# Kernel tuning notes

Hardware: AMD Instinct MI355X
Metric: run time of the kernel (lower is better)

Reference implementation:

```python
import jax, jax.numpy as jnp
import numpy as np

B, N, DIM = 2, 2048, 2048
H, DK, DV = 16, 64, 128
DIM_INNER = (DK + DV) * H  # 3072
EPS = 1e-12  # matches F.normalize clamp_min eps


def l2norm(t):
    n = jnp.linalg.norm(t, axis=-1, keepdims=True)
    return t / jnp.maximum(n, EPS)


def tanh_norm(t):
    n = jnp.linalg.norm(t, axis=-1, keepdims=True)
    return jnp.tanh(n) * (t / jnp.maximum(n, EPS))


def setup_inputs() -> dict:
    key = jax.random.key(0)
    k1, k2, k3, k4 = jax.random.split(key, 4)
    tokens = jax.random.normal(k1, (B, N, DIM), dtype=jnp.float32)
    # Linear weights stored as [in, out] (y = x @ W)
    Wqg = jax.random.normal(k2, (DIM, DIM_INNER), dtype=jnp.float32) * (DIM ** -0.5)
    Wkv = jax.random.normal(k3, (DIM, DIM_INNER), dtype=jnp.float32) * (DIM ** -0.5)
    Wo = jax.random.normal(k4, (DV * H, DIM), dtype=jnp.float32) * ((DV * H) ** -0.5)
    # LearnedScale log_scales, init log(1.0) = 0
    ls_iaw = jnp.zeros((H,), dtype=jnp.float32)  # inverse_acceptance_width (bias=1.0)
    ls_hws = jnp.zeros((H,), dtype=jnp.float32)  # head_wise_scale (bias=0.0)
    return {"tokens": tokens, "Wqg": Wqg, "Wkv": Wkv, "Wo": Wo,
            "ls_iaw": ls_iaw, "ls_hws": ls_hws}


def _split_heads(t):
    # [b, n, h*d] -> [b, h, n, d]
    b, n, _ = t.shape
    return t.reshape(b, n, H, -1).transpose(0, 2, 1, 3)


def reference(tokens, Wqg, Wkv, Wo, ls_iaw, ls_hws):
    qg = _split_heads(tokens @ Wqg)   # [b, h, n, dk+dv]
    kv = _split_heads(tokens @ Wkv)
    queries, gates = qg[..., :DK], qg[..., DK:]
    keys, values = kv[..., :DK], kv[..., DK:]
    queries, keys, values = l2norm(queries), l2norm(keys), l2norm(values)

    sim = jnp.einsum('bhid,bhjd->bhij', queries, keys)
    # r = 1 / (exp(log_scales) + 1)  (LearnedScale bias=1.0)
    r = 1.0 / (jnp.exp(ls_iaw) + 1.0)[None, :, None, None]
    attn = jnp.square(jax.nn.relu(1.0 - r * (1.0 - sim)))
    # NOTE: original code applies causal mask to `sim` AFTER computing `attn`,
    # so the mask has no effect on the output -- replicated faithfully here.
    aggr = jnp.einsum('bhij,bhjd->bhid', attn, values)
    out = tanh_norm(aggr) * jnp.tanh(jax.nn.silu(gates))
    out = out * jnp.exp(ls_hws)[None, :, None, None]  # head_wise_scale, bias=0
    out = out.transpose(0, 2, 1, 3).reshape(tokens.shape[0], tokens.shape[1], H * DV)
    return out @ Wo
```

## Files before the change

### kernel.cpp

```cpp
#include <hip/hip_runtime.h>
#include <hip/hip_bf16.h>
#include <stdint.h>


typedef unsigned short u16;
typedef __bf16 bf16x8 __attribute__((ext_vector_type(8)));
typedef u16 u16x8 __attribute__((ext_vector_type(8)));
typedef float f32x4 __attribute__((ext_vector_type(4)));
typedef float f32x16 __attribute__((ext_vector_type(16)));
typedef int i32x4 __attribute__((ext_vector_type(4)));

#define DEVINL __device__ __forceinline__

DEVINL u16 f2bf(float f) {
  union { float f; uint32_t u; } v; v.f = f;
  uint32_t r = (v.u + 0x7FFFu + ((v.u >> 16) & 1u)) >> 16;
  return (u16)r;
}
DEVINL float bf2f(u16 x) {
  union { uint32_t u; float f; } v; v.u = ((uint32_t)x) << 16;
  return v.f;
}
DEVINL bf16x8 as_bf(u16x8 v) { return __builtin_bit_cast(bf16x8, v); }

typedef const __attribute__((address_space(1))) uint32_t* gptr_t;
typedef __attribute__((address_space(3))) uint32_t* lptr_t;
DEVINL void gload_lds16(const void* g, void* l) {
  __builtin_amdgcn_global_load_lds((gptr_t)g, (lptr_t)l, 16, 0, 0);
}

DEVINL f32x4 mfma16(u16x8 a, u16x8 b, f32x4 c) {
  return __builtin_amdgcn_mfma_f32_16x16x32_bf16(as_bf(a), as_bf(b), c, 0, 0, 0);
}
DEVINL f32x16 mfma32(u16x8 a, u16x8 b, f32x16 c) {
  return __builtin_amdgcn_mfma_f32_32x32x16_bf16(as_bf(a), as_bf(b), c, 0, 0, 0);
}

__global__ void k_cvt(const float* __restrict__ src, u16* __restrict__ dst, int n) {
  int i = (blockIdx.x * blockDim.x + threadIdx.x) * 4;
  int stride = gridDim.x * blockDim.x * 4;
  for (; i < n; i += stride) {
    float4 f = *(const float4*)(src + i);
    ushort4 o;
    o.x = f2bf(f.x); o.y = f2bf(f.y); o.z = f2bf(f.z); o.w = f2bf(f.w);
    *(ushort4*)(dst + i) = o;
  }
}

__global__ void k_cvtT(const float* __restrict__ src, u16* __restrict__ dst, int R, int C) {
  __shared__ float tile[32][33];
  int c0 = blockIdx.x * 32, r0 = blockIdx.y * 32;
  int tc = threadIdx.x & 31, tr = threadIdx.x >> 5;
#pragma unroll
  for (int i = 0; i < 4; i++) {
    int r = tr + i * 8;
    tile[r][tc] = src[(size_t)(r0 + r) * C + c0 + tc];
  }
  __syncthreads();
#pragma unroll
  for (int i = 0; i < 4; i++) {
    int r = tr + i * 8;
    dst[(size_t)(c0 + r) * R + r0 + tc] = f2bf(tile[tc][r]);
  }
}

template <int F32OUT>
__global__ __launch_bounds__(256, 2) void k_gemm(const u16* __restrict__ A,
                                                 const u16* __restrict__ Bt,
                                                 void* __restrict__ Cout,
                                                 int M, int Nt, int K) {
  __shared__ u16 As[128 * 32];
  __shared__ u16 Bs[128 * 32];
  const int tid = threadIdx.x, lane = tid & 63, wid = tid >> 6;
  const int m0 = blockIdx.y * 128, n0 = blockIdx.x * 128;
  const int wm = (wid >> 1) * 64, wn = (wid & 1) * 64;
  const int fr = lane & 15, fc = (lane >> 4) * 8;

  f32x4 acc[4][4] = {};

  const u16* gA = A + (size_t)(m0 + wid * 32 + (lane >> 2)) * K + (lane & 3) * 8;
  const u16* gB = Bt + (size_t)(n0 + wid * 32 + (lane >> 2)) * K + (lane & 3) * 8;
  u16* lA = As + wid * 1024;
  u16* lB = Bs + wid * 1024;
  const size_t rowskip = (size_t)16 * K;

  for (int k0 = 0; k0 < K; k0 += 32) {
    gload_lds16(gA + k0, lA);
    gload_lds16(gA + k0 + rowskip, lA + 512);
    gload_lds16(gB + k0, lB);
    gload_lds16(gB + k0 + rowskip, lB + 512);
    __syncthreads();
    u16x8 a[4], b[4];
#pragma unroll
    for (int mi = 0; mi < 4; mi++) a[mi] = *(const u16x8*)(As + (wm + mi * 16 + fr) * 32 + fc);
#pragma unroll
    for (int ni = 0; ni < 4; ni++) b[ni] = *(const u16x8*)(Bs + (wn + ni * 16 + fr) * 32 + fc);
#pragma unroll
    for (int mi = 0; mi < 4; mi++)
#pragma unroll
      for (int ni = 0; ni < 4; ni++)
        acc[mi][ni] = mfma16(a[mi], b[ni], acc[mi][ni]);
    __syncthreads();
  }

  const int frow = (lane >> 4) * 4;
#pragma unroll
  for (int mi = 0; mi < 4; mi++)
#pragma unroll
    for (int ni = 0; ni < 4; ni++)
#pragma unroll
      for (int j = 0; j < 4; j++) {
        const size_t row = m0 + wm + mi * 16 + frow + j;
        const size_t col = n0 + wn + ni * 16 + fr;
        if (F32OUT) ((float*)Cout)[row * Nt + col] = acc[mi][ni][j];
        else ((u16*)Cout)[row * Nt + col] = f2bf(acc[mi][ni][j]);
      }
}

__global__ __launch_bounds__(256, 4) void k_norm(const u16* __restrict__ qgkv,
                                                 u16* __restrict__ qn, u16* __restrict__ kn,
                                                 u16* __restrict__ vnT, u16* __restrict__ gact) {
  __shared__ u16 vt[128 * 64];
  const int tid = threadIdx.x, lane = tid & 63, wid = tid >> 6;
  const int hb = blockIdx.y;
  const int h = hb & 15, b = hb >> 4;
  const int n0 = blockIdx.x * 64;

  for (int s = 0; s < 16; s++) {
    const int nl = wid * 16 + s;
    const int n = n0 + nl;
    const size_t bn = (size_t)b * 2048 + n;
    const size_t baseq = bn * 6144 + (size_t)h * 192;
    const size_t basek = baseq + 3072;

    float q = bf2f(qgkv[baseq + lane]);
    float g0 = bf2f(qgkv[baseq + 64 + lane]);
    float g1 = bf2f(qgkv[baseq + 128 + lane]);
    float k = bf2f(qgkv[basek + lane]);
    float v0 = bf2f(qgkv[basek + 64 + lane]);
    float v1 = bf2f(qgkv[basek + 128 + lane]);

    float qs = q * q, ks = k * k, vs = v0 * v0 + v1 * v1;
#pragma unroll
    for (int m = 1; m < 64; m <<= 1) {
      qs += __shfl_xor(qs, m);
      ks += __shfl_xor(ks, m);
      vs += __shfl_xor(vs, m);
    }
    float rq = 1.f / fmaxf(sqrtf(qs), 1e-12f);
    float rk = 1.f / fmaxf(sqrtf(ks), 1e-12f);
    float rv = 1.f / fmaxf(sqrtf(vs), 1e-12f);

    qn[((size_t)hb * 2048 + n) * 64 + lane] = f2bf(q * rq);
    kn[((size_t)hb * 2048 + n) * 64 + lane] = f2bf(k * rk);
    float s0 = g0 / (1.f + __expf(-g0));
    float s1 = g1 / (1.f + __expf(-g1));
    gact[((size_t)hb * 2048 + n) * 128 + lane] = f2bf(tanhf(s0));
    gact[((size_t)hb * 2048 + n) * 128 + 64 + lane] = f2bf(tanhf(s1));

    const int d0 = lane, d1 = 64 + lane;
    vt[d0 * 64 + (nl ^ ((d0 & 15) << 2))] = f2bf(v0 * rv);
    vt[d1 * 64 + (nl ^ ((d1 & 15) << 2))] = f2bf(v1 * rv);
  }
  __syncthreads();

#pragma unroll
  for (int p = 0; p < 8; p++) {
    const int d = p * 16 + (tid >> 4);
    const int nq = (tid & 15) * 4;
    const int cb = nq ^ ((d & 15) << 2);
    const int nq2 = (nq & ~12) | ((nq & 4) << 1) | ((nq & 8) >> 1);
    ushort4 o;
    o.x = vt[d * 64 + cb + 0];
    o.y = vt[d * 64 + cb + 1];
    o.z = vt[d * 64 + cb + 2];
    o.w = vt[d * 64 + cb + 3];
    *(ushort4*)(vnT + ((size_t)hb * 128 + d) * 2048 + n0 + nq2) = o;
  }
}

__global__ __launch_bounds__(256, 2) void k_attn(const u16* __restrict__ qn,
                                                 const u16* __restrict__ kn,
                                                 const u16* __restrict__ vnT,
                                                 const u16* __restrict__ gact,
                                                 const float* __restrict__ ls_iaw,
                                                 const float* __restrict__ ls_hws,
                                                 u16* __restrict__ pre_out) {
  extern __shared__ char smem[];
  u16* KsB = (u16*)smem;
  u16* VsB = (u16*)(smem + 16384);
  u16* Os = (u16*)smem;

  const int tid = threadIdx.x, lane = tid & 63, wid = tid >> 6;
  const int bid = blockIdx.y * 16 + blockIdx.x;
  const int bh = (bid & 7) * 4 + ((bid >> 3) & 3);
  const int n0 = (bid >> 5) * 128;
  const int h = bh & 15;
  const int l31 = lane & 31, L = lane >> 5, rb = l31 & 7;
  const float r = 1.f / (__expf(ls_iaw[h]) + 1.f);
  const float c1 = 1.f - r;
  const float whs = __expf(ls_hws[h]);

  const int wq = wid * 32;
  const u16* qrow = qn + ((size_t)bh * 2048 + n0 + wq + l31) * 64;
  u16x8 qf[4];
#pragma unroll
  for (int c = 0; c < 4; c++) qf[c] = *(const u16x8*)(qrow + c * 16 + L * 8);

  f32x16 acc[4] = {};
  const u16* kbase = kn + (size_t)bh * 2048 * 64;
  const u16* vbase = vnT + (size_t)bh * 128 * 2048;

  int ks_goff[2];
#pragma unroll
  for (int i = 0; i < 2; i++) {
    int row = wid * 16 + i * 8 + (lane >> 3);
    ks_goff[i] = row * 64 + (((lane & 7) ^ (row & 7)) << 3);
  }
  int vs_goff[4];
#pragma unroll
  for (int i = 0; i < 4; i++) {
    int row = wid * 32 + i * 8 + (lane >> 3);
    vs_goff[i] = row * 2048 + (((lane & 7) ^ (row & 7)) << 3);
  }

  {
    u16* KsC = KsB + wid * 1024;
    u16* VsC = VsB + wid * 2048;
#pragma unroll
    for (int i = 0; i < 2; i++) gload_lds16(kbase + ks_goff[i], KsC + i * 512);
#pragma unroll
    for (int i = 0; i < 4; i++) gload_lds16(vbase + vs_goff[i], VsC + i * 512);
  }

  int cur = 0;
  for (int t = 0; t < 32; t++) {
    asm volatile("s_waitcnt vmcnt(0) lgkmcnt(0)" ::: "memory");
    __builtin_amdgcn_s_barrier();
    asm volatile("" ::: "memory");

    if (t < 31) {
      const int kv0 = (t + 1) * 64;
      u16* KsC2 = KsB + (cur ^ 1) * 4096 + wid * 1024;
      u16* VsC2 = VsB + (cur ^ 1) * 8192 + wid * 2048;
#pragma unroll
      for (int i = 0; i < 2; i++) gload_lds16(kbase + (size_t)kv0 * 64 + ks_goff[i], KsC2 + i * 512);
#pragma unroll
      for (int i = 0; i < 4; i++) gload_lds16(vbase + (size_t)vs_goff[i] + kv0, VsC2 + i * 512);
    }

    const u16* KsC = KsB + cur * 4096;
    const u16* VsC = VsB + cur * 8192;

    f32x16 sT0 = {}, sT1 = {};
    __builtin_amdgcn_s_setprio(1);
#pragma unroll
    for (int c = 0; c < 4; c++) {
      u16x8 kf0 = *(const u16x8*)(KsC + (0 + l31) * 64 + (((2 * c + L) ^ rb) << 3));
      u16x8 kf1 = *(const u16x8*)(KsC + (32 + l31) * 64 + (((2 * c + L) ^ rb) << 3));
      sT0 = mfma32(kf0, qf[c], sT0);
      sT1 = mfma32(kf1, qf[c], sT1);
    }
    __builtin_amdgcn_s_setprio(0);

    uint32_t w[2][4][2];
#pragma unroll
    for (int m = 0; m < 4; m++)
#pragma unroll
      for (int p = 0; p < 2; p++) {
        float a0 = fmaxf(0.f, fmaf(r, sT0[4 * m + 2 * p], c1));
        float a1 = fmaxf(0.f, fmaf(r, sT0[4 * m + 2 * p + 1], c1));
        float b0 = fmaxf(0.f, fmaf(r, sT1[4 * m + 2 * p], c1));
        float b1 = fmaxf(0.f, fmaf(r, sT1[4 * m + 2 * p + 1], c1));
        w[0][m][p] = (uint32_t)f2bf(a0 * a0) | ((uint32_t)f2bf(a1 * a1) << 16);
        w[1][m][p] = (uint32_t)f2bf(b0 * b0) | ((uint32_t)f2bf(b1 * b1) << 16);
      }

    __builtin_amdgcn_s_setprio(1);
#pragma unroll
    for (int kt = 0; kt < 2; kt++)
#pragma unroll
      for (int pair = 0; pair < 2; pair++) {
        i32x4 pw;
        pw[0] = (int)w[kt][2 * pair][0];
        pw[1] = (int)w[kt][2 * pair][1];
        pw[2] = (int)w[kt][2 * pair + 1][0];
        pw[3] = (int)w[kt][2 * pair + 1][1];
        u16x8 pf = __builtin_bit_cast(u16x8, pw);
        const int chunk = 4 * kt + 2 * pair + L;
#pragma unroll
        for (int dt = 0; dt < 4; dt++) {
          u16x8 vf = *(const u16x8*)(VsC + (dt * 32 + l31) * 64 + ((chunk ^ rb) << 3));
          acc[dt] = mfma32(vf, pf, acc[dt]);
        }
      }
    __builtin_amdgcn_s_setprio(0);
    cur ^= 1;
  }

  float ss = 0.f;
#pragma unroll
  for (int dt = 0; dt < 4; dt++)
#pragma unroll
    for (int e = 0; e < 16; e++) { float x = acc[dt][e]; ss += x * x; }
  ss += __shfl_xor(ss, 32);
  float nn = sqrtf(ss);
  float scale = tanhf(nn) / fmaxf(nn, 1e-12f) * whs;

  __syncthreads();

  const int q = wq + l31;
  const size_t grow = ((size_t)bh * 2048 + n0 + q) * 128;
#pragma unroll
  for (int dt = 0; dt < 4; dt++)
#pragma unroll
    for (int m = 0; m < 4; m++) {
      const int d = dt * 32 + 8 * m + 4 * L;
      ushort4 gv = *(const ushort4*)(gact + grow + d);
      ushort4 o;
      o.x = f2bf(acc[dt][4 * m + 0] * scale * bf2f(gv.x));
      o.y = f2bf(acc[dt][4 * m + 1] * scale * bf2f(gv.y));
      o.z = f2bf(acc[dt][4 * m + 2] * scale * bf2f(gv.z));
      o.w = f2bf(acc[dt][4 * m + 3] * scale * bf2f(gv.w));
      *(ushort4*)(Os + q * 132 + d) = o;
    }
  __syncthreads();

  const int orow = tid >> 1, oc0 = (tid & 1) * 64;
  const size_t obase = ((size_t)(bh >> 4) * 2048 + n0 + orow) * 2048 + (size_t)h * 128 + oc0;
#pragma unroll
  for (int j = 0; j < 16; j++) {
    ushort4 v = *(const ushort4*)(Os + orow * 132 + oc0 + 4 * j);
    *(ushort4*)(pre_out + obase + 4 * j) = v;
  }
}

extern "C" void kernel_launch(void* const* d_in, const int* in_sizes, int n_in,
                              void* d_out, int out_size, void* d_ws, size_t ws_size,
                              hipStream_t stream) {
  (void)in_sizes; (void)n_in; (void)out_size; (void)ws_size;
  const float* tokens = (const float*)d_in[0];
  const float* Wqg = (const float*)d_in[1];
  const float* Wkv = (const float*)d_in[2];
  const float* Wo = (const float*)d_in[3];
  const float* ls_iaw = (const float*)d_in[4];
  const float* ls_hws = (const float*)d_in[5];
  float* out = (float*)d_out;
  char* ws = (char*)d_ws;

  u16* WoT = (u16*)(ws + 0);
  char* regA = ws + 8388608;
  u16* tok_bf = (u16*)(regA);
  u16* WqgkvT = (u16*)(regA + 16777216);
  u16* qn = (u16*)(regA);
  u16* kn = (u16*)(regA + 8388608);
  u16* vnT = (u16*)(regA + 16777216);
  u16* gact = (u16*)(regA + 33554432);
  char* regB = ws + 58720256;
  u16* qgkv_raw = (u16*)(regB);
  u16* pre_out = (u16*)(regB);

  k_cvt<<<4096, 256, 0, stream>>>(tokens, tok_bf, 8388608);
  k_cvtT<<<dim3(96, 64), 256, 0, stream>>>(Wqg, WqgkvT, 2048, 3072);
  k_cvtT<<<dim3(96, 64), 256, 0, stream>>>(Wkv, WqgkvT + (size_t)3072 * 2048, 2048, 3072);
  k_cvtT<<<dim3(64, 64), 256, 0, stream>>>(Wo, WoT, 2048, 2048);

  k_gemm<0><<<dim3(48, 32), 256, 0, stream>>>(tok_bf, WqgkvT, qgkv_raw, 4096, 6144, 2048);

  k_norm<<<dim3(32, 32), 256, 0, stream>>>(qgkv_raw, qn, kn, vnT, gact);

  k_attn<<<dim3(16, 32), 256, 49152, stream>>>(qn, kn, vnT, gact, ls_iaw, ls_hws, pre_out);

  k_gemm<1><<<dim3(16, 32), 256, 0, stream>>>(pre_out, WoT, out, 4096, 2048, 2048);
}
```

Measured before the change: 302.1 us.

## Add 256x256-tile pipelined GEMM for the QG/KV projection

Replaces the QKV projection GEMM with a new kernel that uses 256x256 output tiles, 512 threads and 128 KB of double-buffered LDS. It issues staged direct-to-LDS loads interleaved with quadrant-wise MFMA work, uses a block-index swizzle for L2 locality, and raises wave priority around the MFMA bursts. The larger tiles are meant to raise arithmetic intensity and hide global-load latency behind compute. In exchange, only one block fits per CU and the grid shrinks to 384 blocks, which risks tail imbalance.

```diff
diff --git a/kernel.cpp b/kernel.cpp
--- a/kernel.cpp
+++ b/kernel.cpp
@@ -115,6 +115,118 @@
         if (F32OUT) ((float*)Cout)[row * Nt + col] = acc[mi][ni][j];
         else ((u16*)Cout)[row * Nt + col] = f2bf(acc[mi][ni][j]);
       }
+}
+
+template <int MH, int NH>
+DEVINL void kg_quad(const u16* __restrict__ Ab, const u16* __restrict__ Bb,
+                    f32x4 (&acc)[2][4][2][2], int mq64, int nq32,
+                    int fr, int hi, int rb7) {
+  u16x8 af[4][2], bf[2][2];
+#pragma unroll
+  for (int mi = 0; mi < 4; mi++)
+#pragma unroll
+    for (int kk = 0; kk < 2; kk++) {
+      const int rrow = MH * 128 + mq64 + mi * 16 + fr;
+      af[mi][kk] = *(const u16x8*)(Ab + rrow * 64 + (((kk * 4 + hi) ^ rb7) << 3));
+    }
+#pragma unroll
+  for (int ni = 0; ni < 2; ni++)
+#pragma unroll
+    for (int kk = 0; kk < 2; kk++) {
+      const int rrow = NH * 128 + nq32 + ni * 16 + fr;
+      bf[ni][kk] = *(const u16x8*)(Bb + rrow * 64 + (((kk * 4 + hi) ^ rb7) << 3));
+    }
+  __builtin_amdgcn_s_setprio(1);
+#pragma unroll
+  for (int kk = 0; kk < 2; kk++)
+#pragma unroll
+    for (int mi = 0; mi < 4; mi++)
+#pragma unroll
+      for (int ni = 0; ni < 2; ni++)
+        acc[MH][mi][NH][ni] = mfma16(af[mi][kk], bf[ni][kk], acc[MH][mi][NH][ni]);
+  __builtin_amdgcn_s_setprio(0);
+}
+
+__global__ __launch_bounds__(512, 1) void k_gemm256(const u16* __restrict__ A,
+                                                    const u16* __restrict__ Bt,
+                                                    u16* __restrict__ C,
+                                                    int Nt, int K) {
+  extern __shared__ char smem[];
+  u16* As = (u16*)smem;
+  u16* Bs = (u16*)(smem + 65536);
+  const int tid = threadIdx.x, lane = tid & 63, wid = tid >> 6;
+
+  const int nbx = Nt >> 8;
+  const int cpx = gridDim.x >> 3;
+  const int bid = blockIdx.x;
+  const int swz = (bid & 7) * cpx + (bid >> 3);
+  const int m0 = (swz / nbx) << 8, n0 = (swz % nbx) << 8;
+
+  const int mq64 = (wid >> 2) * 64, nq32 = (wid & 3) * 32;
+  const int fr = lane & 15, hi = lane >> 4, frow = hi * 4, rb7 = fr & 7;
+
+  f32x4 acc[2][4][2][2] = {};
+
+  const int schunk = ((lane & 7) ^ ((lane >> 3) & 7)) << 3;
+  const int srow = wid * 8 + (lane >> 3);
+  const u16* ga0 = A + (size_t)(m0 + srow) * K + schunk;
+  const u16* gb0 = Bt + (size_t)(n0 + srow) * K + schunk;
+  const size_t l64 = (size_t)64 * K;
+  const int dwave = wid * 8 * 64;
+
+#define SA(P, L, KT) gload_lds16(ga0 + (size_t)(L) * l64 + (KT), As + (P) * 16384 + (L) * 4096 + dwave)
+#define SB(P, L, KT) gload_lds16(gb0 + (size_t)(L) * l64 + (KT), Bs + (P) * 16384 + (L) * 4096 + dwave)
+
+  SA(0, 0, 0); SA(0, 1, 0);
+  SB(0, 0, 0); SB(0, 1, 0);
+  SB(0, 2, 0); SB(0, 3, 0);
+  SA(0, 2, 0); SA(0, 3, 0);
+
+  const int NTI = K >> 6;
+  for (int t = 0; t < NTI; t++) {
+    const int p = t & 1, pn = p ^ 1;
+    const int ktn = (t < NTI - 1 ? t + 1 : t) << 6;
+    const u16* Ab = As + p * 16384;
+    const u16* Bb = Bs + p * 16384;
+
+    asm volatile("s_waitcnt vmcnt(4)" ::: "memory");
+    __builtin_amdgcn_s_barrier();
+    asm volatile("" ::: "memory");
+    SA(pn, 0, ktn); SA(pn, 1, ktn);
+    kg_quad<0, 0>(Ab, Bb, acc, mq64, nq32, fr, hi, rb7);
+
+    asm volatile("s_waitcnt vmcnt(4)" ::: "memory");
+    __builtin_amdgcn_s_barrier();
+    asm volatile("" ::: "memory");
+    SB(pn, 0, ktn); SB(pn, 1, ktn);
+    kg_quad<0, 1>(Ab, Bb, acc, mq64, nq32, fr, hi, rb7);
+
+    asm volatile("s_waitcnt vmcnt(4)" ::: "memory");
+    __builtin_amdgcn_s_barrier();
+    asm volatile("" ::: "memory");
+    SB(pn, 2, ktn); SB(pn, 3, ktn);
+    kg_quad<1, 0>(Ab, Bb, acc, mq64, nq32, fr, hi, rb7);
+
+    SA(pn, 2, ktn); SA(pn, 3, ktn);
+    kg_quad<1, 1>(Ab, Bb, acc, mq64, nq32, fr, hi, rb7);
+  }
+#undef SA
+#undef SB
+
+#pragma unroll
+  for (int mh = 0; mh < 2; mh++)
+#pragma unroll
+    for (int mi = 0; mi < 4; mi++)
+#pragma unroll
+      for (int nh = 0; nh < 2; nh++)
+#pragma unroll
+        for (int ni = 0; ni < 2; ni++)
+#pragma unroll
+          for (int j = 0; j < 4; j++) {
+            const size_t row = m0 + mh * 128 + mq64 + mi * 16 + frow + j;
+            const size_t col = n0 + nh * 128 + nq32 + ni * 16 + fr;
+            C[row * Nt + col] = f2bf(acc[mh][mi][nh][ni][j]);
+          }
 }
 
 __global__ __launch_bounds__(256, 4) void k_norm(const u16* __restrict__ qgkv,
@@ -365,7 +477,7 @@
   k_cvtT<<<dim3(96, 64), 256, 0, stream>>>(Wkv, WqgkvT + (size_t)3072 * 2048, 2048, 3072);
   k_cvtT<<<dim3(64, 64), 256, 0, stream>>>(Wo, WoT, 2048, 2048);
 
-  k_gemm<0><<<dim3(48, 32), 256, 0, stream>>>(tok_bf, WqgkvT, qgkv_raw, 4096, 6144, 2048);
+  k_gemm256<<<384, 512, 131072, stream>>>(tok_bf, WqgkvT, qgkv_raw, 6144, 2048);
 
   k_norm<<<dim3(32, 32), 256, 0, stream>>>(qgkv_raw, qn, kn, vnT, gact);
 
```

After: 303.9 us. About the same (+0.6%).

## Replace GEMM with larger-tile triple-buffered pipelined kernel with swizzle and XCD mapping

Applied to the files above, without the earlier changes.

Replaces the single-buffered 128x128 GEMM with a templated 512-thread kernel that uses larger block tiles (256x384 and 128x256). It triple-buffers LDS with async global-to-LDS loads issued two stages ahead, and waits on partial vmcnt. It also XOR-swizzles the LDS layout to reduce bank conflicts, maps blocks to XCDs for L2 locality, and raises wave priority around the MFMA work. Both projection GEMMs now run as one wave of 256 blocks, which costs occupancy and adds register pressure.

```diff
diff --git a/kernel.cpp b/kernel.cpp
--- a/kernel.cpp
+++ b/kernel.cpp
@@ -64,50 +64,95 @@
   }
 }
 
-template <int F32OUT>
-__global__ __launch_bounds__(256, 2) void k_gemm(const u16* __restrict__ A,
-                                                 const u16* __restrict__ Bt,
-                                                 void* __restrict__ Cout,
-                                                 int M, int Nt, int K) {
-  __shared__ u16 As[128 * 32];
-  __shared__ u16 Bs[128 * 32];
+template <int BM, int BN, int WM, int WN, int F32OUT>
+__global__ __launch_bounds__(512, 1) void k_gemm3(const u16* __restrict__ A,
+                                                  const u16* __restrict__ Bt,
+                                                  void* __restrict__ Cout,
+                                                  int M, int Nt, int K) {
+  constexpr int MI = WM / 16, NI = WN / 16;
+  constexpr int NA = BM / 128, NB = BN / 128;
+  constexpr int ABUF = BM * 32, BBUF = BN * 32;
+  extern __shared__ char smem[];
+  u16* As = (u16*)smem;
+  u16* Bs = (u16*)(smem + 3 * ABUF * 2);
+
   const int tid = threadIdx.x, lane = tid & 63, wid = tid >> 6;
-  const int m0 = blockIdx.y * 128, n0 = blockIdx.x * 128;
-  const int wm = (wid >> 1) * 64, wn = (wid & 1) * 64;
-  const int fr = lane & 15, fc = (lane >> 4) * 8;
-
-  f32x4 acc[4][4] = {};
-
-  const u16* gA = A + (size_t)(m0 + wid * 32 + (lane >> 2)) * K + (lane & 3) * 8;
-  const u16* gB = Bt + (size_t)(n0 + wid * 32 + (lane >> 2)) * K + (lane & 3) * 8;
-  u16* lA = As + wid * 1024;
-  u16* lB = Bs + wid * 1024;
-  const size_t rowskip = (size_t)16 * K;
-
-  for (int k0 = 0; k0 < K; k0 += 32) {
-    gload_lds16(gA + k0, lA);
-    gload_lds16(gA + k0 + rowskip, lA + 512);
-    gload_lds16(gB + k0, lB);
-    gload_lds16(gB + k0 + rowskip, lB + 512);
-    __syncthreads();
-    u16x8 a[4], b[4];
-#pragma unroll
-    for (int mi = 0; mi < 4; mi++) a[mi] = *(const u16x8*)(As + (wm + mi * 16 + fr) * 32 + fc);
-#pragma unroll
-    for (int ni = 0; ni < 4; ni++) b[ni] = *(const u16x8*)(Bs + (wn + ni * 16 + fr) * 32 + fc);
-#pragma unroll
-    for (int mi = 0; mi < 4; mi++)
-#pragma unroll
-      for (int ni = 0; ni < 4; ni++)
-        acc[mi][ni] = mfma16(a[mi], b[ni], acc[mi][ni]);
-    __syncthreads();
-  }
-
-  const int frow = (lane >> 4) * 4;
-#pragma unroll
-  for (int mi = 0; mi < 4; mi++)
-#pragma unroll
-    for (int ni = 0; ni < 4; ni++)
+
+  const int NBM = M / BM, NBN = Nt / BN;
+  const int bid = blockIdx.x;
+  const int xcd = bid & 7, idx = bid >> 3;
+  const int m0 = (idx % NBM) * BM;
+  const int n0 = (xcd * (NBN / 8) + idx / NBM) * BN;
+
+  const int wm = (wid >> 2) * WM, wn = (wid & 3) * WN;
+  const int fr = lane & 15, hi = lane >> 4, frow = hi * 4;
+  const int gsw = (hi ^ ((fr >> 1) & 3)) << 3;
+
+  f32x4 acc[MI][NI] = {};
+
+  const int sgran = (((lane & 3) ^ ((lane >> 3) & 3))) << 3;
+  const u16* gA0 = A + (size_t)(m0 + wid * 16 * NA + (lane >> 2)) * K + sgran;
+  const u16* gB0 = Bt + (size_t)(n0 + wid * 16 * NB + (lane >> 2)) * K + sgran;
+  const int adst = wid * 16 * NA * 32;
+  const int bdst = wid * 16 * NB * 32;
+  const size_t r16 = (size_t)16 * K;
+
+#define STAGE(T, S)                                                                  \
+  {                                                                                  \
+    const int kt_ = (T) * 32;                                                        \
+    _Pragma("unroll") for (int i = 0; i < NA; i++)                                   \
+        gload_lds16(gA0 + (size_t)i * r16 + kt_, As + (S)*ABUF + adst + i * 512);    \
+    _Pragma("unroll") for (int i = 0; i < NB; i++)                                   \
+        gload_lds16(gB0 + (size_t)i * r16 + kt_, Bs + (S)*BBUF + bdst + i * 512);    \
+  }
+
+  STAGE(0, 0);
+  STAGE(1, 1);
+
+  const int NTI = K >> 5;
+  int slot = 0;
+  for (int t = 0; t < NTI; t++) {
+    if (t < NTI - 1) {
+      if constexpr (NA + NB == 5) asm volatile("s_waitcnt vmcnt(5)" ::: "memory");
+      else asm volatile("s_waitcnt vmcnt(3)" ::: "memory");
+    } else {
+      asm volatile("s_waitcnt vmcnt(0)" ::: "memory");
+    }
+    asm volatile("s_waitcnt lgkmcnt(0)" ::: "memory");
+    __builtin_amdgcn_s_barrier();
+    asm volatile("" ::: "memory");
+
+    if (t + 2 < NTI) {
+      const int s2 = (slot + 2 >= 3) ? slot - 1 : slot + 2;
+      STAGE(t + 2, s2);
+    }
+
+    const u16* Ab = As + slot * ABUF;
+    const u16* Bb = Bs + slot * BBUF;
+    u16x8 af[MI], bf[NI];
+#pragma unroll
+    for (int mi = 0; mi < MI; mi++)
+      af[mi] = *(const u16x8*)(Ab + (wm + mi * 16 + fr) * 32 + gsw);
+#pragma unroll
+    for (int ni = 0; ni < NI; ni++)
+      bf[ni] = *(const u16x8*)(Bb + (wn + ni * 16 + fr) * 32 + gsw);
+
+    __builtin_amdgcn_s_setprio(1);
+#pragma unroll
+    for (int mi = 0; mi < MI; mi++)
+#pragma unroll
+      for (int ni = 0; ni < NI; ni++)
+        acc[mi][ni] = mfma16(af[mi], bf[ni], acc[mi][ni]);
+    __builtin_amdgcn_s_setprio(0);
+
+    slot = (slot + 1 >= 3) ? 0 : slot + 1;
+  }
+#undef STAGE
+
+#pragma unroll
+  for (int mi = 0; mi < MI; mi++)
+#pragma unroll
+    for (int ni = 0; ni < NI; ni++)
 #pragma unroll
       for (int j = 0; j < 4; j++) {
         const size_t row = m0 + wm + mi * 16 + frow + j;
@@ -365,11 +410,11 @@
   k_cvtT<<<dim3(96, 64), 256, 0, stream>>>(Wkv, WqgkvT + (size_t)3072 * 2048, 2048, 3072);
   k_cvtT<<<dim3(64, 64), 256, 0, stream>>>(Wo, WoT, 2048, 2048);
 
-  k_gemm<0><<<dim3(48, 32), 256, 0, stream>>>(tok_bf, WqgkvT, qgkv_raw, 4096, 6144, 2048);
+  k_gemm3<256, 384, 128, 96, 0><<<256, 512, 122880, stream>>>(tok_bf, WqgkvT, qgkv_raw, 4096, 6144, 2048);
 
   k_norm<<<dim3(32, 32), 256, 0, stream>>>(qgkv_raw, qn, kn, vnT, gact);
 
   k_attn<<<dim3(16, 32), 256, 49152, stream>>>(qn, kn, vnT, gact, ls_iaw, ls_hws, pre_out);
 
-  k_gemm<1><<<dim3(16, 32), 256, 0, stream>>>(pre_out, WoT, out, 4096, 2048, 2048);
-}
+  k_gemm3<128, 256, 64, 64, 1><<<256, 512, 73728, stream>>>(pre_out, WoT, out, 4096, 2048, 2048);
+}
```

Result: slower. 312.5 us (+3.4%).

## Replace GEMM with larger-tile double-buffered LDS GEMM with swizzle and XCD mapping

Applied to the files above, without the earlier changes.

Replaces the 128x128 single-buffered GEMM with a 512-thread kernel using 128x384 or 128x256 tiles and K-step 64. It double-buffers LDS, prefetching the next tile while computing the current one, and XOR-swizzles LDS chunks to avoid bank conflicts. Blocks are mapped across the XCDs for L2 locality, and MFMA priority is raised. The larger tiles need much more dynamic LDS and one block per CU, which lowers occupancy.

```diff
diff --git a/kernel.cpp b/kernel.cpp
--- a/kernel.cpp
+++ b/kernel.cpp
@@ -64,57 +64,114 @@
   }
 }
 
-template <int F32OUT>
-__global__ __launch_bounds__(256, 2) void k_gemm(const u16* __restrict__ A,
-                                                 const u16* __restrict__ Bt,
-                                                 void* __restrict__ Cout,
-                                                 int M, int Nt, int K) {
-  __shared__ u16 As[128 * 32];
-  __shared__ u16 Bs[128 * 32];
+template <int NI, int F32OUT>
+__global__ __launch_bounds__(512, 1) void k_gemmU(const u16* __restrict__ A,
+                                                  const u16* __restrict__ Bt,
+                                                  void* __restrict__ Cout,
+                                                  int Nt, int K) {
+  constexpr int BN = NI * 128;
+  constexpr int NLB = BN / 64;
+  constexpr int ABUF = 128 * 64;
+  constexpr int BBUF = BN * 64;
+  extern __shared__ char smem[];
+  u16* As = (u16*)smem;
+  u16* Bs = (u16*)(smem + 2 * ABUF * 2);
+
   const int tid = threadIdx.x, lane = tid & 63, wid = tid >> 6;
-  const int m0 = blockIdx.y * 128, n0 = blockIdx.x * 128;
-  const int wm = (wid >> 1) * 64, wn = (wid & 1) * 64;
-  const int fr = lane & 15, fc = (lane >> 4) * 8;
-
-  f32x4 acc[4][4] = {};
-
-  const u16* gA = A + (size_t)(m0 + wid * 32 + (lane >> 2)) * K + (lane & 3) * 8;
-  const u16* gB = Bt + (size_t)(n0 + wid * 32 + (lane >> 2)) * K + (lane & 3) * 8;
-  u16* lA = As + wid * 1024;
-  u16* lB = Bs + wid * 1024;
-  const size_t rowskip = (size_t)16 * K;
-
-  for (int k0 = 0; k0 < K; k0 += 32) {
-    gload_lds16(gA + k0, lA);
-    gload_lds16(gA + k0 + rowskip, lA + 512);
-    gload_lds16(gB + k0, lB);
-    gload_lds16(gB + k0 + rowskip, lB + 512);
-    __syncthreads();
-    u16x8 a[4], b[4];
-#pragma unroll
-    for (int mi = 0; mi < 4; mi++) a[mi] = *(const u16x8*)(As + (wm + mi * 16 + fr) * 32 + fc);
-#pragma unroll
-    for (int ni = 0; ni < 4; ni++) b[ni] = *(const u16x8*)(Bs + (wn + ni * 16 + fr) * 32 + fc);
-#pragma unroll
-    for (int mi = 0; mi < 4; mi++)
-#pragma unroll
-      for (int ni = 0; ni < 4; ni++)
-        acc[mi][ni] = mfma16(a[mi], b[ni], acc[mi][ni]);
-    __syncthreads();
-  }
-
-  const int frow = (lane >> 4) * 4;
-#pragma unroll
-  for (int mi = 0; mi < 4; mi++)
-#pragma unroll
-    for (int ni = 0; ni < 4; ni++)
-#pragma unroll
-      for (int j = 0; j < 4; j++) {
-        const size_t row = m0 + wm + mi * 16 + frow + j;
-        const size_t col = n0 + wn + ni * 16 + fr;
-        if (F32OUT) ((float*)Cout)[row * Nt + col] = acc[mi][ni][j];
-        else ((u16*)Cout)[row * Nt + col] = f2bf(acc[mi][ni][j]);
-      }
+
+  const int NPN = Nt / BN;
+  const int bid = blockIdx.x;
+  const int xcd = bid & 7, idx = bid >> 3;
+  const int npx = NPN >> 3;
+  const int m0 = (idx & 31) * 128;
+  const int n0 = (xcd * npx + (idx >> 5)) * BN;
+
+  const int mq = (wid >> 2) * 32, nq = (wid & 3) * (BN / 8);
+  const int fr = lane & 15, hi = lane >> 4, frow = hi * 4, rb7 = fr & 7;
+
+  f32x4 acc[2][2][2][NI] = {};
+
+  const int schunk = ((lane & 7) ^ ((lane >> 3) & 7)) << 3;
+  const int srow = wid * 8 + (lane >> 3);
+  const u16* ga0 = A + (size_t)(m0 + srow) * K + schunk;
+  const u16* gb0 = Bt + (size_t)(n0 + srow) * K + schunk;
+  const size_t l64 = (size_t)64 * K;
+  const int dwave = wid * 512;
+
+#define STG(T, P)                                                                     \
+  {                                                                                   \
+    const int kt_ = (T) << 6;                                                         \
+    _Pragma("unroll") for (int i = 0; i < 2; i++)                                     \
+        gload_lds16(ga0 + (size_t)i * l64 + kt_, As + (P) * ABUF + i * 4096 + dwave); \
+    _Pragma("unroll") for (int i = 0; i < NLB; i++)                                   \
+        gload_lds16(gb0 + (size_t)i * l64 + kt_, Bs + (P) * BBUF + i * 4096 + dwave); \
+  }
+
+  STG(0, 0);
+
+  const int NTI = K >> 6;
+  for (int t = 0; t < NTI; t++) {
+    asm volatile("s_waitcnt vmcnt(0) lgkmcnt(0)" ::: "memory");
+    __builtin_amdgcn_s_barrier();
+    asm volatile("" ::: "memory");
+
+    const int p = t & 1;
+    if (t + 1 < NTI) STG(t + 1, p ^ 1);
+
+    const u16* Ab = As + p * ABUF;
+    const u16* Bb = Bs + p * BBUF;
+
+    u16x8 af[2][2][2], bf[2][NI][2];
+#pragma unroll
+    for (int MH = 0; MH < 2; MH++)
+#pragma unroll
+      for (int mi = 0; mi < 2; mi++)
+#pragma unroll
+        for (int kk = 0; kk < 2; kk++) {
+          const int row = MH * 64 + mq + mi * 16 + fr;
+          af[MH][mi][kk] = *(const u16x8*)(Ab + row * 64 + (((kk * 4 + hi) ^ rb7) << 3));
+        }
+#pragma unroll
+    for (int NH = 0; NH < 2; NH++)
+#pragma unroll
+      for (int ni = 0; ni < NI; ni++)
+#pragma unroll
+        for (int kk = 0; kk < 2; kk++) {
+          const int row = NH * (BN / 2) + nq + ni * 16 + fr;
+          bf[NH][ni][kk] = *(const u16x8*)(Bb + row * 64 + (((kk * 4 + hi) ^ rb7) << 3));
+        }
+
+    __builtin_amdgcn_s_setprio(1);
+#pragma unroll
+    for (int kk = 0; kk < 2; kk++)
+#pragma unroll
+      for (int MH = 0; MH < 2; MH++)
+#pragma unroll
+        for (int mi = 0; mi < 2; mi++)
+#pragma unroll
+          for (int NH = 0; NH < 2; NH++)
+#pragma unroll
+            for (int ni = 0; ni < NI; ni++)
+              acc[MH][mi][NH][ni] = mfma16(af[MH][mi][kk], bf[NH][ni][kk], acc[MH][mi][NH][ni]);
+    __builtin_amdgcn_s_setprio(0);
+  }
+#undef STG
+
+#pragma unroll
+  for (int MH = 0; MH < 2; MH++)
+#pragma unroll
+    for (int mi = 0; mi < 2; mi++)
+#pragma unroll
+      for (int NH = 0; NH < 2; NH++)
+#pragma unroll
+        for (int ni = 0; ni < NI; ni++)
+#pragma unroll
+          for (int j = 0; j < 4; j++) {
+            const size_t row = m0 + MH * 64 + mq + mi * 16 + frow + j;
+            const size_t col = n0 + NH * (BN / 2) + nq + ni * 16 + fr;
+            if (F32OUT) ((float*)Cout)[row * Nt + col] = acc[MH][mi][NH][ni][j];
+            else ((u16*)Cout)[row * Nt + col] = f2bf(acc[MH][mi][NH][ni][j]);
+          }
 }
 
 __global__ __launch_bounds__(256, 4) void k_norm(const u16* __restrict__ qgkv,
@@ -365,11 +422,11 @@
   k_cvtT<<<dim3(96, 64), 256, 0, stream>>>(Wkv, WqgkvT + (size_t)3072 * 2048, 2048, 3072);
   k_cvtT<<<dim3(64, 64), 256, 0, stream>>>(Wo, WoT, 2048, 2048);
 
-  k_gemm<0><<<dim3(48, 32), 256, 0, stream>>>(tok_bf, WqgkvT, qgkv_raw, 4096, 6144, 2048);
+  k_gemmU<3, 0><<<512, 512, 131072, stream>>>(tok_bf, WqgkvT, qgkv_raw, 6144, 2048);
 
   k_norm<<<dim3(32, 32), 256, 0, stream>>>(qgkv_raw, qn, kn, vnT, gact);
 
   k_attn<<<dim3(16, 32), 256, 49152, stream>>>(qn, kn, vnT, gact, ls_iaw, ls_hws, pre_out);
 
-  k_gemm<1><<<dim3(16, 32), 256, 0, stream>>>(pre_out, WoT, out, 4096, 2048, 2048);
-}
+  k_gemmU<2, 1><<<256, 512, 98304, stream>>>(pre_out, WoT, out, 2048, 2048);
+}
```

Result: faster. 272.3 us (-9.9%).
